# Optimization experiments

Measured on AMD Instinct MI355X. Metric: run time of the kernel, lower is better.

## Reference

```python
import jax, jax.numpy as jnp
import numpy as np

H = 8  # heads hardcoded in LightGFormer


def layernorm(x, g, b, eps=1e-5):
    m = x.mean(-1, keepdims=True)
    v = ((x - m) ** 2).mean(-1, keepdims=True)
    return (x - m) / jnp.sqrt(v + eps) * g + b


def setup_inputs() -> dict:
    key = jax.random.key(0)
    B, N, D, L = 16, 512, 256, 4
    Dff = 4 * D
    ks = jax.random.split(key, 12)

    def w(k, shape, scale=0.02):
        return jax.random.normal(k, shape, jnp.float32) * scale

    return {
        "input": w(ks[0], (B, N, D), 1.0),
        "input_v": w(ks[1], (B, N, D), 1.0),
        "pos_emb": w(ks[2], (N, D)),
        "Wq": w(ks[3], (L, D, D)), "bq": jnp.zeros((L, D), jnp.float32),
        "Wk": w(ks[4], (L, D, D)), "bk": jnp.zeros((L, D), jnp.float32),
        "Wv": w(ks[5], (L, D, D)), "bv": jnp.zeros((L, D), jnp.float32),
        "Wo": w(ks[6], (L, D, D)), "bo": jnp.zeros((L, D), jnp.float32),
        "W1": w(ks[7], (L, D, Dff)), "b1": jnp.zeros((L, Dff), jnp.float32),
        "W2": w(ks[8], (L, Dff // 2, D // 2)), "b2": jnp.zeros((L, D // 2), jnp.float32),
        "g1": jnp.ones((L, D), jnp.float32), "be1": jnp.zeros((L, D), jnp.float32),
        "g2": jnp.ones((L, D), jnp.float32), "be2": jnp.zeros((L, D), jnp.float32),
        "gf": jnp.ones((D,), jnp.float32), "bf": jnp.zeros((D,), jnp.float32),
        "mask": jax.random.randint(ks[9], (N, N), 0, 2) > 0,
    }


def reference(input, input_v, pos_emb, Wq, bq, Wk, bk, Wv, bv, Wo, bo,
              W1, b1, W2, b2, g1, be1, g2, be2, gf, bf, mask):
    B, N, D = input.shape
    L = Wq.shape[0]
    dk = D // H
    scale = 1.0 / float(np.sqrt(dk))

    x = input + pos_emb[None]       # learned positional encoding
    xv = input_v + pos_emb[None]    # values stream (never updated across layers)

    for i in range(L):
        # --- self-attention: queries/keys from x, values from xv ---
        q = (x @ Wq[i] + bq[i]).reshape(B, N, H, dk)
        k = (x @ Wk[i] + bk[i]).reshape(B, N, H, dk)
        v = (xv @ Wv[i] + bv[i]).reshape(B, N, H, dk)
        att = jnp.einsum('bqhd,bkhd->bhqk', q, k) * scale
        if i % 2 == 1:  # odd layers use the mask (Lightformer alternation)
            att = jnp.where(mask[None, None], -jnp.inf, att)
        att = jax.nn.softmax(att, axis=-1)
        o = jnp.einsum('bhqk,bkhd->bqhd', att, v).reshape(B, N, D)
        o = o @ Wo[i] + bo[i]
        x = layernorm(x + o, g1[i], be1[i])
        # --- FFN with grouped second linear: [.., 2, 2D] @ [2D, D/2] ---
        h = jax.nn.gelu(x @ W1[i] + b1[i], approximate=False)
        h = (h.reshape(B, N, 2, 2 * D) @ W2[i] + b2[i]).reshape(B, N, D)
        x = layernorm(x + h, g2[i], be2[i])

    x = layernorm(x, gf, bf)  # final attention_norm
    return x
```

## Files before the change

### kernel.cpp

```cpp
#include <hip/hip_runtime.h>
#include <hip/hip_bf16.h>
#include <math.h>

#define BDIM 16
#define NSEQ 512
#define DMODEL 256
#define NLAYER 4
#define NHEAD 8
#define DK 32
#define DFF 1024
#define BN (BDIM * NSEQ)
#define ND (NSEQ * DMODEL)

typedef __bf16 bf16x8 __attribute__((ext_vector_type(8)));
typedef float floatx4 __attribute__((ext_vector_type(4)));
typedef unsigned uint32x2 __attribute__((ext_vector_type(2)));

static __device__ __forceinline__ unsigned short f2bf(float f) {
    unsigned u = __float_as_uint(f);
    unsigned r = (u + 0x7FFFu + ((u >> 16) & 1u)) >> 16;
    return (unsigned short)r;
}

static __device__ __forceinline__ void async_ld16(const unsigned short* g,
                                                  unsigned short* l) {
    __builtin_amdgcn_global_load_lds(
        (const __attribute__((address_space(1))) unsigned int*)g,
        (__attribute__((address_space(3))) unsigned int*)l, 16, 0, 0);
}

static __device__ __forceinline__ float gelu_f(float c) {
    float u = 0.7978845608028654f * (c + 0.044715f * c * c * c);
    return c * (1.f / (1.f + __expf(-2.f * u)));
}

__global__ void conv_all_kernel(const float* __restrict__ Wq, const float* __restrict__ Wk,
                                const float* __restrict__ Wv, const float* __restrict__ Wo,
                                const float* __restrict__ W1, const float* __restrict__ W2,
                                const int* __restrict__ mask,
                                unsigned short* __restrict__ wqT, unsigned short* __restrict__ wkT,
                                unsigned short* __restrict__ wvT, unsigned short* __restrict__ woT,
                                unsigned short* __restrict__ w1T, unsigned short* __restrict__ w2T,
                                unsigned* __restrict__ bits) {
    int blk = blockIdx.x, tid = threadIdx.x;
    if (blk < 4096) {
        int i = blk * 256 + tid;
        int sel = i >> 18;
        int j = i & 262143;
        int l = j >> 16, rem = j & 65535, kk = rem >> 8, n = rem & 255;
        const float* src = sel == 0 ? Wq : sel == 1 ? Wk : sel == 2 ? Wv : Wo;
        unsigned short* dst = sel == 0 ? wqT : sel == 1 ? wkT : sel == 2 ? wvT : woT;
        dst[(size_t)l * 65536 + n * 256 + kk] = f2bf(src[j]);
    } else if (blk < 8192) {
        int i = (blk - 4096) * 256 + tid;
        int l = i >> 18, rem = i & 262143, kk = rem >> 10, n = rem & 1023;
        w1T[(size_t)l * 262144 + (size_t)n * 256 + kk] = f2bf(W1[i]);
    } else if (blk < 9216) {
        int j = (blk - 8192) * 256 + tid;
        int l = j >> 16, rem = j & 65535, kk = rem >> 7, n = rem & 127;
        w2T[(size_t)l * 65536 + (size_t)n * 512 + kk] = f2bf(W2[j]);
    } else {
        int w = (blk - 9216) * 256 + tid;
        int r = w >> 4, wi = w & 15;
        const int* src = mask + r * NSEQ + wi * 32;
        unsigned acc = 0;
#pragma unroll
        for (int j = 0; j < 32; j++) acc |= (src[j] != 0 ? 1u : 0u) << j;
        bits[w] = acc;
    }
}

__global__ void add_pos_kernel(const float* __restrict__ in,
                               const float* __restrict__ inv,
                               const float* __restrict__ pos,
                               float* __restrict__ x,
                               unsigned short* __restrict__ xb,
                               unsigned short* __restrict__ xvb,
                               int total) {
    int i = blockIdx.x * blockDim.x + threadIdx.x;
    if (i < total) {
        float pe = pos[i % ND];
        float a = in[i] + pe;
        float b = inv[i] + pe;
        x[i] = a;
        xb[i] = f2bf(a);
        xvb[i] = f2bf(b);
    }
}

__global__ __launch_bounds__(256) void qkv_mfma_kernel(
        const unsigned short* __restrict__ xb,
        const unsigned short* __restrict__ xvb,
        const unsigned short* __restrict__ WqT, const unsigned short* __restrict__ WkT,
        const unsigned short* __restrict__ WvT,
        const float* __restrict__ bq, const float* __restrict__ bk,
        const float* __restrict__ bv,
        unsigned short* __restrict__ qo, unsigned short* __restrict__ ko,
        unsigned short* __restrict__ vo) {
    int proj = blockIdx.x >> 1;
    const unsigned short* A  = (proj == 2) ? xvb : xb;
    const unsigned short* Bt = (proj == 0) ? WqT : (proj == 1) ? WkT : WvT;
    const float* bias        = (proj == 0) ? bq  : (proj == 1) ? bk  : bv;
    unsigned short* Cb       = (proj == 0) ? qo  : (proj == 1) ? ko  : vo;
    float qscale = (proj == 0) ? 0.17677669529663687f : 1.f;

    __shared__ unsigned short As[2][128 * 32];
    __shared__ unsigned short Bs[2][128 * 32];
    int tid = threadIdx.x;
    int wave = tid >> 6, lane = tid & 63;
    int rowBase = blockIdx.y * 128, colBase = (blockIdx.x & 1) * 128;
    int m0w = (wave & 1) * 64, n0w = (wave >> 1) * 64;
    int lr = lane & 15, quad = lane >> 4;
    int qx = quad ^ (lr & 3);

    floatx4 acc[4][4];
#pragma unroll
    for (int mi = 0; mi < 4; mi++)
#pragma unroll
        for (int nj = 0; nj < 4; nj++) acc[mi][nj] = (floatx4)0.0f;

    auto stage = [&](int kt, int b) {
#pragma unroll
        for (int t = 0; t < 2; t++) {
            int idx = t * 256 + tid;
            int row = idx >> 2, kv8 = ((idx ^ row) & 3) * 8;
            async_ld16(A + (size_t)(rowBase + row) * DMODEL + kt * 32 + kv8, &As[b][idx * 8]);
            async_ld16(Bt + (size_t)(colBase + row) * DMODEL + kt * 32 + kv8, &Bs[b][idx * 8]);
        }
    };
    stage(0, 0);

    for (int kt = 0; kt < 8; kt++) {
        int cur = kt & 1;
        bool more = (kt < 7);
        if (more) stage(kt + 1, cur ^ 1);
        if (more) asm volatile("s_waitcnt vmcnt(4)");
        else      asm volatile("s_waitcnt vmcnt(0)");
        __builtin_amdgcn_s_barrier();
        __builtin_amdgcn_sched_barrier(0);
        bf16x8 af[4], bfr[4];
#pragma unroll
        for (int mi = 0; mi < 4; mi++)
            af[mi] = *(const bf16x8*)&As[cur][(m0w + mi * 16 + lr) * 32 + qx * 8];
#pragma unroll
        for (int nj = 0; nj < 4; nj++)
            bfr[nj] = *(const bf16x8*)&Bs[cur][(n0w + nj * 16 + lr) * 32 + qx * 8];
#pragma unroll
        for (int mi = 0; mi < 4; mi++)
#pragma unroll
            for (int nj = 0; nj < 4; nj++)
                acc[mi][nj] = __builtin_amdgcn_mfma_f32_16x16x32_bf16(
                    af[mi], bfr[nj], acc[mi][nj], 0, 0, 0);
        if (more) {
            asm volatile("s_waitcnt lgkmcnt(0)");
            __builtin_amdgcn_sched_barrier(0);
            __builtin_amdgcn_s_barrier();
        }
    }

#pragma unroll
    for (int mi = 0; mi < 4; mi++) {
#pragma unroll
        for (int r = 0; r < 4; r++) {
            int grow = rowBase + m0w + mi * 16 + quad * 4 + r;
#pragma unroll
            for (int nj = 0; nj < 4; nj++) {
                int gcol = colBase + n0w + nj * 16 + lr;
                float c = (acc[mi][nj][r] + bias[gcol]) * qscale;
                size_t off = ((size_t)((grow >> 9) * 8 + (gcol >> 5)) << 14)
                           + (size_t)(grow & 511) * 32 + (gcol & 31);
                Cb[off] = f2bf(c);
            }
        }
    }
}

__global__ __launch_bounds__(256) void gemm_mfma_kernel(
        const unsigned short* __restrict__ A,
        const unsigned short* __restrict__ Bt,
        const float* __restrict__ bias,
        unsigned short* __restrict__ Cb,
        int M, int K, int N, int act) {
    __shared__ unsigned short As[2][128 * 32];
    __shared__ unsigned short Bs[2][128 * 32];
    int tid = threadIdx.x;
    int wave = tid >> 6, lane = tid & 63;
    int rowBase = blockIdx.y * 128, colBase = blockIdx.x * 128;
    int m0w = (wave & 1) * 64, n0w = (wave >> 1) * 64;
    int lr = lane & 15, quad = lane >> 4;
    int qx = quad ^ (lr & 3);
    int NK = K >> 5;

    floatx4 acc[4][4];
#pragma unroll
    for (int mi = 0; mi < 4; mi++)
#pragma unroll
        for (int nj = 0; nj < 4; nj++) acc[mi][nj] = (floatx4)0.0f;

    auto stage = [&](int kt, int b) {
#pragma unroll
        for (int t = 0; t < 2; t++) {
            int idx = t * 256 + tid;
            int row = idx >> 2, kv8 = ((idx ^ row) & 3) * 8;
            async_ld16(A + (size_t)(rowBase + row) * K + kt * 32 + kv8, &As[b][idx * 8]);
            async_ld16(Bt + (size_t)(colBase + row) * K + kt * 32 + kv8, &Bs[b][idx * 8]);
        }
    };
    stage(0, 0);

    for (int kt = 0; kt < NK; kt++) {
        int cur = kt & 1;
        bool more = (kt < NK - 1);
        if (more) stage(kt + 1, cur ^ 1);
        if (more) asm volatile("s_waitcnt vmcnt(4)");
        else      asm volatile("s_waitcnt vmcnt(0)");
        __builtin_amdgcn_s_barrier();
        __builtin_amdgcn_sched_barrier(0);
        bf16x8 af[4], bfr[4];
#pragma unroll
        for (int mi = 0; mi < 4; mi++)
            af[mi] = *(const bf16x8*)&As[cur][(m0w + mi * 16 + lr) * 32 + qx * 8];
#pragma unroll
        for (int nj = 0; nj < 4; nj++)
            bfr[nj] = *(const bf16x8*)&Bs[cur][(n0w + nj * 16 + lr) * 32 + qx * 8];
#pragma unroll
        for (int mi = 0; mi < 4; mi++)
#pragma unroll
            for (int nj = 0; nj < 4; nj++)
                acc[mi][nj] = __builtin_amdgcn_mfma_f32_16x16x32_bf16(
                    af[mi], bfr[nj], acc[mi][nj], 0, 0, 0);
        if (more) {
            asm volatile("s_waitcnt lgkmcnt(0)");
            __builtin_amdgcn_sched_barrier(0);
            __builtin_amdgcn_s_barrier();
        }
    }

#pragma unroll
    for (int mi = 0; mi < 4; mi++) {
#pragma unroll
        for (int r = 0; r < 4; r++) {
            int grow = rowBase + m0w + mi * 16 + quad * 4 + r;
#pragma unroll
            for (int nj = 0; nj < 4; nj++) {
                int gcol = colBase + n0w + nj * 16 + lr;
                float c = acc[mi][nj][r] + bias[gcol];
                if (act) c = gelu_f(c);
                Cb[(size_t)grow * N + gcol] = f2bf(c);
            }
        }
    }
}

__global__ __launch_bounds__(64) void wo_ln_kernel(
        const unsigned short* __restrict__ A,
        const unsigned short* __restrict__ Bt,
        const float* __restrict__ bias,
        const float* __restrict__ g, const float* __restrict__ be,
        float* __restrict__ xf, unsigned short* __restrict__ xb) {
    __shared__ unsigned short As[2][16 * 32];
    __shared__ unsigned short Bs[2][256 * 32];
    int tid = threadIdx.x;
    int l16 = tid & 15, quad = tid >> 4;
    int rowBase = blockIdx.x * 16;
    int qx = quad ^ (l16 & 3);

    floatx4 acc[16];
#pragma unroll
    for (int t = 0; t < 16; t++) acc[t] = (floatx4)0.0f;

    auto stage = [&](int kt, int b) {
        {
            int row = tid >> 2, kv8 = ((tid ^ row) & 3) * 8;
            async_ld16(A + (size_t)(rowBase + row) * 256 + kt * 32 + kv8, &As[b][tid * 8]);
        }
#pragma unroll
        for (int t = 0; t < 16; t++) {
            int idx = t * 64 + tid;
            int row = idx >> 2, kv8 = ((idx ^ row) & 3) * 8;
            async_ld16(Bt + (size_t)row * 256 + kt * 32 + kv8, &Bs[b][idx * 8]);
        }
    };
    stage(0, 0);

    for (int kt = 0; kt < 8; kt++) {
        int cur = kt & 1;
        bool more = (kt < 7);
        if (more) stage(kt + 1, cur ^ 1);
        if (more) asm volatile("s_waitcnt vmcnt(17)");
        else      asm volatile("s_waitcnt vmcnt(0)");
        __builtin_amdgcn_sched_barrier(0);
        bf16x8 af = *(const bf16x8*)&As[cur][l16 * 32 + qx * 8];
#pragma unroll
        for (int t = 0; t < 16; t++) {
            bf16x8 bfr = *(const bf16x8*)&Bs[cur][(t * 16 + l16) * 32 + qx * 8];
            acc[t] = __builtin_amdgcn_mfma_f32_16x16x32_bf16(af, bfr, acc[t], 0, 0, 0);
        }
    }

    float bcol[16], gc[16], bec[16];
#pragma unroll
    for (int t = 0; t < 16; t++) {
        int c = t * 16 + l16;
        bcol[t] = bias[c]; gc[t] = g[c]; bec[t] = be[c];
    }
#pragma unroll
    for (int r = 0; r < 4; r++) {
        int grow = rowBase + quad * 4 + r;
        float v[16], s = 0.f, s2 = 0.f;
#pragma unroll
        for (int t = 0; t < 16; t++) {
            int c = t * 16 + l16;
            float val = acc[t][r] + bcol[t] + xf[(size_t)grow * 256 + c];
            v[t] = val; s += val; s2 += val * val;
        }
#pragma unroll
        for (int off = 1; off <= 8; off <<= 1) {
            s += __shfl_xor(s, off);
            s2 += __shfl_xor(s2, off);
        }
        float mean = s * (1.f / 256.f);
        float var = s2 * (1.f / 256.f) - mean * mean;
        float rstd = rsqrtf(var + 1e-5f);
#pragma unroll
        for (int t = 0; t < 16; t++) {
            int c = t * 16 + l16;
            float o = (v[t] - mean) * rstd * gc[t] + bec[t];
            xf[(size_t)grow * 256 + c] = o;
            xb[(size_t)grow * 256 + c] = f2bf(o);
        }
    }
}

__global__ __launch_bounds__(128) void ffn2_ln_kernel(
        const unsigned short* __restrict__ A,
        const unsigned short* __restrict__ Bt,
        const float* __restrict__ bias,
        const float* __restrict__ g, const float* __restrict__ be,
        float* __restrict__ xf, unsigned short* __restrict__ xb) {
    __shared__ unsigned short As[2][64 * 32];
    __shared__ unsigned short Bs[2][128 * 32];
    __shared__ float redS[64][2], redQ[64][2];
    int tid = threadIdx.x;
    int wave = tid >> 6, lane = tid & 63, l16 = lane & 15, quad = lane >> 4;
    int rowBase = blockIdx.x * 64;
    int n0w = wave * 64;
    int qx = quad ^ (l16 & 3);

    floatx4 acc[4][4];
#pragma unroll
    for (int mi = 0; mi < 4; mi++)
#pragma unroll
        for (int nj = 0; nj < 4; nj++) acc[mi][nj] = (floatx4)0.0f;

    auto stage = [&](int kt, int b) {
#pragma unroll
        for (int t = 0; t < 2; t++) {
            int idx = t * 128 + tid;
            int row = idx >> 2, kv8 = ((idx ^ row) & 3) * 8;
            async_ld16(A + (size_t)(rowBase + row) * 512 + kt * 32 + kv8, &As[b][idx * 8]);
        }
#pragma unroll
        for (int t = 0; t < 4; t++) {
            int idx = t * 128 + tid;
            int row = idx >> 2, kv8 = ((idx ^ row) & 3) * 8;
            async_ld16(Bt + (size_t)row * 512 + kt * 32 + kv8, &Bs[b][idx * 8]);
        }
    };
    stage(0, 0);

    for (int kt = 0; kt < 16; kt++) {
        int cur = kt & 1;
        bool more = (kt < 15);
        if (more) stage(kt + 1, cur ^ 1);
        if (more) asm volatile("s_waitcnt vmcnt(6)");
        else      asm volatile("s_waitcnt vmcnt(0)");
        __builtin_amdgcn_s_barrier();
        __builtin_amdgcn_sched_barrier(0);
        bf16x8 af[4], bfr[4];
#pragma unroll
        for (int mi = 0; mi < 4; mi++)
            af[mi] = *(const bf16x8*)&As[cur][(mi * 16 + l16) * 32 + qx * 8];
#pragma unroll
        for (int nj = 0; nj < 4; nj++)
            bfr[nj] = *(const bf16x8*)&Bs[cur][(n0w + nj * 16 + l16) * 32 + qx * 8];
#pragma unroll
        for (int mi = 0; mi < 4; mi++)
#pragma unroll
            for (int nj = 0; nj < 4; nj++)
                acc[mi][nj] = __builtin_amdgcn_mfma_f32_16x16x32_bf16(
                    af[mi], bfr[nj], acc[mi][nj], 0, 0, 0);
        if (more) {
            asm volatile("s_waitcnt lgkmcnt(0)");
            __builtin_amdgcn_sched_barrier(0);
            __builtin_amdgcn_s_barrier();
        }
    }

#pragma unroll
    for (int mi = 0; mi < 4; mi++) {
#pragma unroll
        for (int r = 0; r < 4; r++) {
            int row = mi * 16 + quad * 4 + r;
            int grow = rowBase + row;
            int token = grow >> 1, dbase = (grow & 1) * 128;
            float s = 0.f, s2 = 0.f;
#pragma unroll
            for (int nj = 0; nj < 4; nj++) {
                int gcol = n0w + nj * 16 + l16;
                float val = acc[mi][nj][r] + bias[gcol]
                          + xf[(size_t)token * 256 + dbase + gcol];
                acc[mi][nj][r] = val;
                s += val; s2 += val * val;
            }
#pragma unroll
            for (int off = 1; off <= 8; off <<= 1) {
                s += __shfl_xor(s, off);
                s2 += __shfl_xor(s2, off);
            }
            if (l16 == 0) { redS[row][wave] = s; redQ[row][wave] = s2; }
        }
    }
    __syncthreads();

#pragma unroll
    for (int mi = 0; mi < 4; mi++) {
#pragma unroll
        for (int r = 0; r < 4; r++) {
            int row = mi * 16 + quad * 4 + r;
            int grow = rowBase + row;
            int token = grow >> 1, dbase = (grow & 1) * 128;
            float ts = redS[row][0] + redS[row][1] + redS[row ^ 1][0] + redS[row ^ 1][1];
            float tq = redQ[row][0] + redQ[row][1] + redQ[row ^ 1][0] + redQ[row ^ 1][1];
            float mean = ts * (1.f / 256.f);
            float var = tq * (1.f / 256.f) - mean * mean;
            float rstd = rsqrtf(var + 1e-5f);
#pragma unroll
            for (int nj = 0; nj < 4; nj++) {
                int gcol = n0w + nj * 16 + l16;
                int d = dbase + gcol;
                float o = (acc[mi][nj][r] - mean) * rstd * g[d] + be[d];
                xf[(size_t)token * 256 + d] = o;
                xb[(size_t)token * 256 + d] = f2bf(o);
            }
        }
    }
}

__global__ __launch_bounds__(256, 4) void attn_mfma_kernel(
        const unsigned short* __restrict__ q, const unsigned short* __restrict__ k,
        const unsigned short* __restrict__ v, unsigned short* __restrict__ o,
        const unsigned* __restrict__ mbits_g, int use_mask) {
    int bid = blockIdx.x;
    int qg = bid >> 7;
    int bh = bid & 127;
    int h = bh & 7, b = bh >> 3;
    int tid = threadIdx.x;

    __shared__ unsigned short Vs[2][NSEQ * 16];

    const unsigned short* kbase = k + (size_t)(b * 8 + h) * (NSEQ * DK);
    const unsigned short* vbase = v + (size_t)(b * 8 + h) * (NSEQ * DK);

#pragma unroll
    for (int db = 0; db < 2; db++) {
#pragma unroll
        for (int t = 0; t < 4; t++) {
            int c = t * 256 + tid;
            int kk = c >> 1, half = c & 1;
            async_ld16(vbase + (size_t)kk * 32 + db * 16 + half * 8,
                       &Vs[db][c * 8]);
        }
    }

    int wave = tid >> 6, lane = tid & 63, l16 = lane & 15, quad = lane >> 4;
    int qbase = qg * 64 + wave * 16;

    bf16x8 qf = *(const bf16x8*)(q + ((size_t)(b * 8 + h) * NSEQ + qbase + l16) * 32 + quad * 8);

    unsigned mw[16];
    if (use_mask) {
        const uint4* mr = (const uint4*)(mbits_g + (size_t)(qbase + l16) * 16);
#pragma unroll
        for (int w = 0; w < 4; w++) *(uint4*)&mw[w * 4] = mr[w];
    } else {
#pragma unroll
        for (int w = 0; w < 16; w++) mw[w] = 0;
    }
    __syncthreads();

    unsigned va0 = (unsigned)(size_t)&Vs[0][0] + (unsigned)(lane * 8);
    unsigned va1 = (unsigned)(size_t)&Vs[1][0] + (unsigned)(lane * 8);

    const unsigned short* kfrag = kbase + (size_t)l16 * DK + quad * 8;

    floatx4 oT0 = (floatx4)0.f, oT1 = (floatx4)0.f;
    float m_run = -INFINITY, l_part = 0.f;

    uint32x2 t00, t01, t10, t11;
#define TR_ISSUE(cc)                                                      \
    asm volatile("ds_read_b64_tr_b16 %0, %4\n\t"                          \
                 "ds_read_b64_tr_b16 %1, %4 offset:512\n\t"               \
                 "ds_read_b64_tr_b16 %2, %5\n\t"                          \
                 "ds_read_b64_tr_b16 %3, %5 offset:512"                   \
                 : "=&v"(t00), "=&v"(t01), "=&v"(t10), "=&v"(t11)         \
                 : "v"(va0 + (unsigned)((cc) * 1024)),                    \
                   "v"(va1 + (unsigned)((cc) * 1024)))
    TR_ISSUE(0);

    bf16x8 k0 = *(const bf16x8*)(kfrag);
    bf16x8 k1 = *(const bf16x8*)(kfrag + 16 * DK);

#pragma unroll
    for (int c = 0; c < 16; c++) {
        floatx4 s0 = __builtin_amdgcn_mfma_f32_16x16x32_bf16(k0, qf, (floatx4)0.f, 0, 0, 0);
        floatx4 s1 = __builtin_amdgcn_mfma_f32_16x16x32_bf16(k1, qf, (floatx4)0.f, 0, 0, 0);

        bf16x8 k0n, k1n;
        if (c < 15) {
            k0n = *(const bf16x8*)(kfrag + (size_t)((c + 1) * 32) * DK);
            k1n = *(const bf16x8*)(kfrag + (size_t)((c + 1) * 32 + 16) * DK);
        }

        float sv[8];
#pragma unroll
        for (int r = 0; r < 4; r++) { sv[r] = s0[r]; sv[4 + r] = s1[r]; }
        if (use_mask) {
            unsigned wb = mw[c];
#pragma unroll
            for (int r = 0; r < 4; r++) {
                if ((wb >> (quad * 4 + r)) & 1) sv[r] = -INFINITY;
                if ((wb >> (16 + quad * 4 + r)) & 1) sv[4 + r] = -INFINITY;
            }
        }
        float mx = fmaxf(fmaxf(fmaxf(sv[0], sv[1]), fmaxf(sv[2], sv[3])),
                         fmaxf(fmaxf(sv[4], sv[5]), fmaxf(sv[6], sv[7])));
        mx = fmaxf(mx, __shfl_xor(mx, 16));
        mx = fmaxf(mx, __shfl_xor(mx, 32));
        if (!__all(mx <= m_run)) {
            float mnew = fmaxf(m_run, mx);
            float corr = (m_run == mnew) ? 1.f : __expf(m_run - mnew);
            l_part *= corr;
            oT0 *= corr; oT1 *= corr;
            m_run = mnew;
        }
        float p[8];
#pragma unroll
        for (int j = 0; j < 8; j++) {
            float e = __expf(sv[j] - m_run);
            p[j] = (sv[j] > -INFINITY) ? e : 0.f;
            l_part += p[j];
        }
        union { bf16x8 v8; unsigned u[4]; } pf;
#pragma unroll
        for (int j = 0; j < 4; j++)
            asm("v_cvt_pk_bf16_f32 %0, %1, %2"
                : "=v"(pf.u[j]) : "v"(p[2 * j]), "v"(p[2 * j + 1]));

        asm volatile("s_waitcnt lgkmcnt(0)");
        __builtin_amdgcn_sched_barrier(0);
        union { bf16x8 v8; uint32x2 u[2]; } av0, av1;
        av0.u[0] = t00; av0.u[1] = t01;
        av1.u[0] = t10; av1.u[1] = t11;

        oT0 = __builtin_amdgcn_mfma_f32_16x16x32_bf16(av0.v8, pf.v8, oT0, 0, 0, 0);
        oT1 = __builtin_amdgcn_mfma_f32_16x16x32_bf16(av1.v8, pf.v8, oT1, 0, 0, 0);
        if (c < 15) TR_ISSUE(c + 1);
        k0 = k0n; k1 = k1n;
    }
#undef TR_ISSUE

    float l = l_part;
    l += __shfl_xor(l, 16);
    l += __shfl_xor(l, 32);
    float invl = (l > 0.f) ? 1.f / l : 0.f;

    unsigned short* orow = o + ((size_t)(b * NSEQ + qbase + l16)) * DMODEL + h * DK;
#pragma unroll
    for (int r = 0; r < 4; r++) {
        orow[quad * 4 + r]      = f2bf(oT0[r] * invl);
        orow[16 + quad * 4 + r] = f2bf(oT1[r] * invl);
    }
}

__global__ __launch_bounds__(256) void final_ln_kernel(
        const float* __restrict__ a,
        const float* __restrict__ g, const float* __restrict__ be,
        float* __restrict__ out) {
    int t = blockIdx.x;
    int d = threadIdx.x;
    size_t idx = (size_t)t * DMODEL + d;
    float v = a[idx];
    float s = v, s2 = v * v;
#pragma unroll
    for (int off = 32; off; off >>= 1) {
        s  += __shfl_xor(s, off);
        s2 += __shfl_xor(s2, off);
    }
    __shared__ float ws1[4], ws2[4];
    int wid = d >> 6;
    if ((d & 63) == 0) { ws1[wid] = s; ws2[wid] = s2; }
    __syncthreads();
    s  = ws1[0] + ws1[1] + ws1[2] + ws1[3];
    s2 = ws2[0] + ws2[1] + ws2[2] + ws2[3];
    float mean = s * (1.f / DMODEL);
    float var = s2 * (1.f / DMODEL) - mean * mean;
    float rstd = rsqrtf(var + 1e-5f);
    out[idx] = (v - mean) * rstd * g[d] + be[d];
}

extern "C" void kernel_launch(void* const* d_in, const int* in_sizes, int n_in,
                              void* d_out, int out_size, void* d_ws, size_t ws_size,
                              hipStream_t stream) {
    const float* input  = (const float*)d_in[0];
    const float* inputv = (const float*)d_in[1];
    const float* pos    = (const float*)d_in[2];
    const float* Wq = (const float*)d_in[3];
    const float* bq = (const float*)d_in[4];
    const float* Wk = (const float*)d_in[5];
    const float* bk = (const float*)d_in[6];
    const float* Wv = (const float*)d_in[7];
    const float* bv = (const float*)d_in[8];
    const float* Wo = (const float*)d_in[9];
    const float* bo = (const float*)d_in[10];
    const float* W1 = (const float*)d_in[11];
    const float* b1 = (const float*)d_in[12];
    const float* W2 = (const float*)d_in[13];
    const float* b2 = (const float*)d_in[14];
    const float* g1 = (const float*)d_in[15];
    const float* be1 = (const float*)d_in[16];
    const float* g2 = (const float*)d_in[17];
    const float* be2 = (const float*)d_in[18];
    const float* gf = (const float*)d_in[19];
    const float* bff = (const float*)d_in[20];
    const int* mask = (const int*)d_in[21];

    float* out = (float*)d_out;

    char* wsb = (char*)d_ws;
    float* x_f  = (float*)(wsb + ((size_t)0 << 20));
    unsigned short* x_b  = (unsigned short*)(wsb + ((size_t)8 << 20));
    unsigned short* xv_b = (unsigned short*)(wsb + ((size_t)12 << 20));
    unsigned short* qb_b = (unsigned short*)(wsb + ((size_t)16 << 20));
    unsigned short* kb_b = (unsigned short*)(wsb + ((size_t)20 << 20));
    unsigned short* vb_b = (unsigned short*)(wsb + ((size_t)24 << 20));
    unsigned short* ab_b = (unsigned short*)(wsb + ((size_t)28 << 20));
    unsigned short* h_b  = qb_b;
    unsigned short* wqT = (unsigned short*)(wsb + ((size_t)32 << 20));
    unsigned short* wkT = wqT + (size_t)4 * 65536;
    unsigned short* wvT = wkT + (size_t)4 * 65536;
    unsigned short* woT = wvT + (size_t)4 * 65536;
    unsigned short* w1T = woT + (size_t)4 * 65536;
    unsigned short* w2T = w1T + (size_t)4 * 262144;
    unsigned* mbits = (unsigned*)(wsb + ((size_t)37 << 20));

    const size_t TOK = (size_t)BN * DMODEL;

    conv_all_kernel<<<9248, 256, 0, stream>>>(Wq, Wk, Wv, Wo, W1, W2, mask,
                                              wqT, wkT, wvT, woT, w1T, w2T, mbits);
    add_pos_kernel<<<(int)((TOK + 255) / 256), 256, 0, stream>>>(
        input, inputv, pos, x_f, x_b, xv_b, (int)TOK);

    for (int i = 0; i < NLAYER; i++) {
        const unsigned short* WqT_i = wqT + (size_t)i * 65536;
        const unsigned short* WkT_i = wkT + (size_t)i * 65536;
        const unsigned short* WvT_i = wvT + (size_t)i * 65536;
        const unsigned short* WoT_i = woT + (size_t)i * 65536;
        const unsigned short* W1T_i = w1T + (size_t)i * 262144;
        const unsigned short* W2T_i = w2T + (size_t)i * 65536;

        qkv_mfma_kernel<<<dim3(6, 64), 256, 0, stream>>>(
            x_b, xv_b, WqT_i, WkT_i, WvT_i,
            bq + i * DMODEL, bk + i * DMODEL, bv + i * DMODEL,
            qb_b, kb_b, vb_b);

        attn_mfma_kernel<<<BDIM * NHEAD * 8, 256, 0, stream>>>(
            qb_b, kb_b, vb_b, ab_b, mbits, (i & 1));

        wo_ln_kernel<<<BN / 16, 64, 0, stream>>>(
            ab_b, WoT_i, bo + i * DMODEL,
            g1 + i * DMODEL, be1 + i * DMODEL, x_f, x_b);

        gemm_mfma_kernel<<<dim3(8, 64), 256, 0, stream>>>(
            x_b, W1T_i, b1 + i * DFF, h_b, BN, DMODEL, DFF, 1);

        ffn2_ln_kernel<<<(2 * BN) / 64, 128, 0, stream>>>(
            h_b, W2T_i, b2 + i * (DMODEL / 2),
            g2 + i * DMODEL, be2 + i * DMODEL, x_f, x_b);
    }

    final_ln_kernel<<<BN, DMODEL, 0, stream>>>(x_f, gf, bff, out);
}
```

Measured before the change: 462.4 us.

## Fuse Wo+LN1, FFN1+GELU, FFN2+LN2 and final LN into one per-layer kernel

Replaces the Wo+LayerNorm kernel, the FFN1 GEMM with GELU, and the grouped FFN2+LayerNorm kernel with a single kernel per layer. Each block handles 32 tokens and keeps the post-attention activations and the 1024-wide hidden layer in LDS, so the hidden tensor is never written to or read from global memory. The final LayerNorm is folded into the last layer's epilogue. In exchange, each block streams every weight matrix for only 32 rows, which lowers weight reuse, and the large LDS footprint with only 256 blocks may limit occupancy.

```diff
diff --git a/kernel.cpp b/kernel.cpp
--- a/kernel.cpp
+++ b/kernel.cpp
@@ -20,6 +20,9 @@
     unsigned u = __float_as_uint(f);
     unsigned r = (u + 0x7FFFu + ((u >> 16) & 1u)) >> 16;
     return (unsigned short)r;
+}
+static __device__ __forceinline__ float bf2f(unsigned short u) {
+    return __uint_as_float(((unsigned)u) << 16);
 }
 
 static __device__ __forceinline__ void async_ld16(const unsigned short* g,
@@ -175,275 +178,353 @@
     }
 }
 
-__global__ __launch_bounds__(256) void gemm_mfma_kernel(
-        const unsigned short* __restrict__ A,
-        const unsigned short* __restrict__ Bt,
-        const float* __restrict__ bias,
-        unsigned short* __restrict__ Cb,
-        int M, int K, int N, int act) {
-    __shared__ unsigned short As[2][128 * 32];
-    __shared__ unsigned short Bs[2][128 * 32];
+__global__ __launch_bounds__(256) void ffn_fused_kernel(
+        const unsigned short* __restrict__ Aab,
+        const unsigned short* __restrict__ woT,
+        const unsigned short* __restrict__ w1T,
+        const unsigned short* __restrict__ w2T,
+        const float* __restrict__ bo,
+        const float* __restrict__ g1, const float* __restrict__ be1,
+        const float* __restrict__ b1,
+        const float* __restrict__ b2,
+        const float* __restrict__ g2, const float* __restrict__ be2,
+        const float* __restrict__ gf, const float* __restrict__ bf_,
+        float* __restrict__ xf, unsigned short* __restrict__ xb,
+        float* __restrict__ outF, int finalize) {
+    __shared__ unsigned short Ab[8][1024];
+    __shared__ unsigned short X1[8][1024];
+    __shared__ unsigned short Hh[16][1024];
+    __shared__ unsigned short Bst[16384];
+    __shared__ float redA[32][4], redB[32][4];
+    __shared__ float redC[32][4], redD[32][4];
+    __shared__ float redE[32][4], redF[32][4];
+
     int tid = threadIdx.x;
-    int wave = tid >> 6, lane = tid & 63;
-    int rowBase = blockIdx.y * 128, colBase = blockIdx.x * 128;
-    int m0w = (wave & 1) * 64, n0w = (wave >> 1) * 64;
-    int lr = lane & 15, quad = lane >> 4;
-    int qx = quad ^ (lr & 3);
-    int NK = K >> 5;
-
-    floatx4 acc[4][4];
-#pragma unroll
-    for (int mi = 0; mi < 4; mi++)
-#pragma unroll
-        for (int nj = 0; nj < 4; nj++) acc[mi][nj] = (floatx4)0.0f;
-
-    auto stage = [&](int kt, int b) {
-#pragma unroll
-        for (int t = 0; t < 2; t++) {
-            int idx = t * 256 + tid;
-            int row = idx >> 2, kv8 = ((idx ^ row) & 3) * 8;
-            async_ld16(A + (size_t)(rowBase + row) * K + kt * 32 + kv8, &As[b][idx * 8]);
-            async_ld16(Bt + (size_t)(colBase + row) * K + kt * 32 + kv8, &Bs[b][idx * 8]);
+    int w = tid >> 6, lane = tid & 63, l16 = lane & 15, quad = lane >> 4;
+    int qx = quad ^ (l16 & 3);
+    int rowBase = blockIdx.x * 32;
+    unsigned short* Bw = Bst + w * 4096;
+
+    float b1r[2][4][2];
+#pragma unroll
+    for (int g = 0; g < 2; g++)
+#pragma unroll
+        for (int nc = 0; nc < 4; nc++)
+#pragma unroll
+            for (int cj = 0; cj < 2; cj++) {
+                b1r[g][nc][cj] = b1[g * 512 + w * 128 + nc * 32 + cj * 16 + l16];
+                asm volatile("" :: "v"(b1r[g][nc][cj]));
+            }
+
+#pragma unroll
+    for (int t = 0; t < 4; t++) {
+        int idx = t * 256 + tid;
+        int kt = idx >> 7;
+        int r  = (idx >> 2) & 31;
+        int ch = idx & 3, chx = ch ^ (r & 3);
+        async_ld16(Aab + (size_t)(rowBase + r) * 256 + kt * 32 + chx * 8,
+                   ((unsigned short*)Ab) + idx * 8);
+    }
+
+    floatx4 accA[2][4];
+#pragma unroll
+    for (int mi = 0; mi < 2; mi++)
+#pragma unroll
+        for (int nj = 0; nj < 4; nj++) accA[mi][nj] = (floatx4)0.0f;
+
+    auto stageA = [&](int kt, int b) {
+#pragma unroll
+        for (int t = 0; t < 4; t++) {
+            int idx = t * 64 + lane;
+            int r = idx >> 2, ch = idx & 3, chx = ch ^ (r & 3);
+            async_ld16(woT + (size_t)(w * 64 + r) * 256 + kt * 32 + chx * 8,
+                       Bw + b * 2048 + idx * 8);
         }
     };
-    stage(0, 0);
-
-    for (int kt = 0; kt < NK; kt++) {
+    stageA(0, 0);
+    stageA(1, 1);
+    asm volatile("s_waitcnt vmcnt(4)");
+    __builtin_amdgcn_sched_barrier(0);
+    __builtin_amdgcn_s_barrier();
+    __builtin_amdgcn_sched_barrier(0);
+
+#pragma unroll
+    for (int kt = 0; kt < 8; kt++) {
         int cur = kt & 1;
-        bool more = (kt < NK - 1);
-        if (more) stage(kt + 1, cur ^ 1);
-        if (more) asm volatile("s_waitcnt vmcnt(4)");
-        else      asm volatile("s_waitcnt vmcnt(0)");
-        __builtin_amdgcn_s_barrier();
+        if (kt < 7) asm volatile("s_waitcnt vmcnt(4)");
+        else        asm volatile("s_waitcnt vmcnt(0)");
         __builtin_amdgcn_sched_barrier(0);
-        bf16x8 af[4], bfr[4];
-#pragma unroll
-        for (int mi = 0; mi < 4; mi++)
-            af[mi] = *(const bf16x8*)&As[cur][(m0w + mi * 16 + lr) * 32 + qx * 8];
+        bf16x8 af[2], bfr[4];
+#pragma unroll
+        for (int mi = 0; mi < 2; mi++)
+            af[mi] = *(const bf16x8*)&Ab[kt][(mi * 16 + l16) * 32 + qx * 8];
 #pragma unroll
         for (int nj = 0; nj < 4; nj++)
-            bfr[nj] = *(const bf16x8*)&Bs[cur][(n0w + nj * 16 + lr) * 32 + qx * 8];
-#pragma unroll
-        for (int mi = 0; mi < 4; mi++)
+            bfr[nj] = *(const bf16x8*)(Bw + cur * 2048 + (nj * 16 + l16) * 32 + qx * 8);
+#pragma unroll
+        for (int mi = 0; mi < 2; mi++)
 #pragma unroll
             for (int nj = 0; nj < 4; nj++)
-                acc[mi][nj] = __builtin_amdgcn_mfma_f32_16x16x32_bf16(
-                    af[mi], bfr[nj], acc[mi][nj], 0, 0, 0);
-        if (more) {
+                accA[mi][nj] = __builtin_amdgcn_mfma_f32_16x16x32_bf16(
+                    af[mi], bfr[nj], accA[mi][nj], 0, 0, 0);
+        if (kt < 6) {
             asm volatile("s_waitcnt lgkmcnt(0)");
             __builtin_amdgcn_sched_barrier(0);
-            __builtin_amdgcn_s_barrier();
-        }
-    }
-
-#pragma unroll
-    for (int mi = 0; mi < 4; mi++) {
-#pragma unroll
-        for (int r = 0; r < 4; r++) {
-            int grow = rowBase + m0w + mi * 16 + quad * 4 + r;
-#pragma unroll
-            for (int nj = 0; nj < 4; nj++) {
-                int gcol = colBase + n0w + nj * 16 + lr;
-                float c = acc[mi][nj][r] + bias[gcol];
-                if (act) c = gelu_f(c);
-                Cb[(size_t)grow * N + gcol] = f2bf(c);
-            }
-        }
-    }
-}
-
-__global__ __launch_bounds__(64) void wo_ln_kernel(
-        const unsigned short* __restrict__ A,
-        const unsigned short* __restrict__ Bt,
-        const float* __restrict__ bias,
-        const float* __restrict__ g, const float* __restrict__ be,
-        float* __restrict__ xf, unsigned short* __restrict__ xb) {
-    __shared__ unsigned short As[2][16 * 32];
-    __shared__ unsigned short Bs[2][256 * 32];
-    int tid = threadIdx.x;
-    int l16 = tid & 15, quad = tid >> 4;
-    int rowBase = blockIdx.x * 16;
-    int qx = quad ^ (l16 & 3);
-
-    floatx4 acc[16];
-#pragma unroll
-    for (int t = 0; t < 16; t++) acc[t] = (floatx4)0.0f;
-
-    auto stage = [&](int kt, int b) {
-        {
-            int row = tid >> 2, kv8 = ((tid ^ row) & 3) * 8;
-            async_ld16(A + (size_t)(rowBase + row) * 256 + kt * 32 + kv8, &As[b][tid * 8]);
-        }
-#pragma unroll
-        for (int t = 0; t < 16; t++) {
-            int idx = t * 64 + tid;
-            int row = idx >> 2, kv8 = ((idx ^ row) & 3) * 8;
-            async_ld16(Bt + (size_t)row * 256 + kt * 32 + kv8, &Bs[b][idx * 8]);
-        }
-    };
-    stage(0, 0);
-
-    for (int kt = 0; kt < 8; kt++) {
-        int cur = kt & 1;
-        bool more = (kt < 7);
-        if (more) stage(kt + 1, cur ^ 1);
-        if (more) asm volatile("s_waitcnt vmcnt(17)");
-        else      asm volatile("s_waitcnt vmcnt(0)");
-        __builtin_amdgcn_sched_barrier(0);
-        bf16x8 af = *(const bf16x8*)&As[cur][l16 * 32 + qx * 8];
-#pragma unroll
-        for (int t = 0; t < 16; t++) {
-            bf16x8 bfr = *(const bf16x8*)&Bs[cur][(t * 16 + l16) * 32 + qx * 8];
-            acc[t] = __builtin_amdgcn_mfma_f32_16x16x32_bf16(af, bfr, acc[t], 0, 0, 0);
-        }
-    }
-
-    float bcol[16], gc[16], bec[16];
-#pragma unroll
-    for (int t = 0; t < 16; t++) {
-        int c = t * 16 + l16;
-        bcol[t] = bias[c]; gc[t] = g[c]; bec[t] = be[c];
-    }
-#pragma unroll
-    for (int r = 0; r < 4; r++) {
-        int grow = rowBase + quad * 4 + r;
-        float v[16], s = 0.f, s2 = 0.f;
-#pragma unroll
-        for (int t = 0; t < 16; t++) {
-            int c = t * 16 + l16;
-            float val = acc[t][r] + bcol[t] + xf[(size_t)grow * 256 + c];
-            v[t] = val; s += val; s2 += val * val;
-        }
-#pragma unroll
-        for (int off = 1; off <= 8; off <<= 1) {
-            s += __shfl_xor(s, off);
-            s2 += __shfl_xor(s2, off);
-        }
-        float mean = s * (1.f / 256.f);
-        float var = s2 * (1.f / 256.f) - mean * mean;
-        float rstd = rsqrtf(var + 1e-5f);
-#pragma unroll
-        for (int t = 0; t < 16; t++) {
-            int c = t * 16 + l16;
-            float o = (v[t] - mean) * rstd * gc[t] + bec[t];
-            xf[(size_t)grow * 256 + c] = o;
-            xb[(size_t)grow * 256 + c] = f2bf(o);
-        }
-    }
-}
-
-__global__ __launch_bounds__(128) void ffn2_ln_kernel(
-        const unsigned short* __restrict__ A,
-        const unsigned short* __restrict__ Bt,
-        const float* __restrict__ bias,
-        const float* __restrict__ g, const float* __restrict__ be,
-        float* __restrict__ xf, unsigned short* __restrict__ xb) {
-    __shared__ unsigned short As[2][64 * 32];
-    __shared__ unsigned short Bs[2][128 * 32];
-    __shared__ float redS[64][2], redQ[64][2];
-    int tid = threadIdx.x;
-    int wave = tid >> 6, lane = tid & 63, l16 = lane & 15, quad = lane >> 4;
-    int rowBase = blockIdx.x * 64;
-    int n0w = wave * 64;
-    int qx = quad ^ (l16 & 3);
-
-    floatx4 acc[4][4];
-#pragma unroll
-    for (int mi = 0; mi < 4; mi++)
-#pragma unroll
-        for (int nj = 0; nj < 4; nj++) acc[mi][nj] = (floatx4)0.0f;
-
-    auto stage = [&](int kt, int b) {
-#pragma unroll
-        for (int t = 0; t < 2; t++) {
-            int idx = t * 128 + tid;
-            int row = idx >> 2, kv8 = ((idx ^ row) & 3) * 8;
-            async_ld16(A + (size_t)(rowBase + row) * 512 + kt * 32 + kv8, &As[b][idx * 8]);
-        }
-#pragma unroll
-        for (int t = 0; t < 4; t++) {
-            int idx = t * 128 + tid;
-            int row = idx >> 2, kv8 = ((idx ^ row) & 3) * 8;
-            async_ld16(Bt + (size_t)row * 512 + kt * 32 + kv8, &Bs[b][idx * 8]);
-        }
-    };
-    stage(0, 0);
-
-    for (int kt = 0; kt < 16; kt++) {
-        int cur = kt & 1;
-        bool more = (kt < 15);
-        if (more) stage(kt + 1, cur ^ 1);
-        if (more) asm volatile("s_waitcnt vmcnt(6)");
-        else      asm volatile("s_waitcnt vmcnt(0)");
-        __builtin_amdgcn_s_barrier();
-        __builtin_amdgcn_sched_barrier(0);
-        bf16x8 af[4], bfr[4];
-#pragma unroll
-        for (int mi = 0; mi < 4; mi++)
-            af[mi] = *(const bf16x8*)&As[cur][(mi * 16 + l16) * 32 + qx * 8];
-#pragma unroll
-        for (int nj = 0; nj < 4; nj++)
-            bfr[nj] = *(const bf16x8*)&Bs[cur][(n0w + nj * 16 + l16) * 32 + qx * 8];
-#pragma unroll
-        for (int mi = 0; mi < 4; mi++)
-#pragma unroll
-            for (int nj = 0; nj < 4; nj++)
-                acc[mi][nj] = __builtin_amdgcn_mfma_f32_16x16x32_bf16(
-                    af[mi], bfr[nj], acc[mi][nj], 0, 0, 0);
-        if (more) {
-            asm volatile("s_waitcnt lgkmcnt(0)");
-            __builtin_amdgcn_sched_barrier(0);
-            __builtin_amdgcn_s_barrier();
-        }
-    }
-
-#pragma unroll
-    for (int mi = 0; mi < 4; mi++) {
+            stageA(kt + 2, cur);
+        }
+    }
+
+#pragma unroll
+    for (int mi = 0; mi < 2; mi++)
 #pragma unroll
         for (int r = 0; r < 4; r++) {
             int row = mi * 16 + quad * 4 + r;
-            int grow = rowBase + row;
-            int token = grow >> 1, dbase = (grow & 1) * 128;
             float s = 0.f, s2 = 0.f;
 #pragma unroll
             for (int nj = 0; nj < 4; nj++) {
-                int gcol = n0w + nj * 16 + l16;
-                float val = acc[mi][nj][r] + bias[gcol]
-                          + xf[(size_t)token * 256 + dbase + gcol];
-                acc[mi][nj][r] = val;
-                s += val; s2 += val * val;
+                int col = w * 64 + nj * 16 + l16;
+                float v = accA[mi][nj][r] + bo[col]
+                        + xf[(size_t)(rowBase + row) * 256 + col];
+                accA[mi][nj][r] = v; s += v; s2 += v * v;
             }
 #pragma unroll
             for (int off = 1; off <= 8; off <<= 1) {
                 s += __shfl_xor(s, off);
                 s2 += __shfl_xor(s2, off);
             }
-            if (l16 == 0) { redS[row][wave] = s; redQ[row][wave] = s2; }
-        }
-    }
+            if (l16 == 0) { redA[row][w] = s; redB[row][w] = s2; }
+        }
     __syncthreads();
-
-#pragma unroll
-    for (int mi = 0; mi < 4; mi++) {
+#pragma unroll
+    for (int mi = 0; mi < 2; mi++)
 #pragma unroll
         for (int r = 0; r < 4; r++) {
             int row = mi * 16 + quad * 4 + r;
-            int grow = rowBase + row;
-            int token = grow >> 1, dbase = (grow & 1) * 128;
-            float ts = redS[row][0] + redS[row][1] + redS[row ^ 1][0] + redS[row ^ 1][1];
-            float tq = redQ[row][0] + redQ[row][1] + redQ[row ^ 1][0] + redQ[row ^ 1][1];
+            float ts = redA[row][0] + redA[row][1] + redA[row][2] + redA[row][3];
+            float tq = redB[row][0] + redB[row][1] + redB[row][2] + redB[row][3];
             float mean = ts * (1.f / 256.f);
             float var = tq * (1.f / 256.f) - mean * mean;
             float rstd = rsqrtf(var + 1e-5f);
 #pragma unroll
             for (int nj = 0; nj < 4; nj++) {
-                int gcol = n0w + nj * 16 + l16;
-                int d = dbase + gcol;
-                float o = (acc[mi][nj][r] - mean) * rstd * g[d] + be[d];
-                xf[(size_t)token * 256 + d] = o;
-                xb[(size_t)token * 256 + d] = f2bf(o);
-            }
-        }
+                int col = w * 64 + nj * 16 + l16;
+                float o = (accA[mi][nj][r] - mean) * rstd * g1[col] + be1[col];
+                int c5 = col & 31;
+                X1[col >> 5][row * 32 + (((c5 >> 3) ^ (row & 3)) << 3) + (c5 & 7)] = f2bf(o);
+            }
+        }
+    __syncthreads();
+
+    floatx4 y[2][2][2];
+#pragma unroll
+    for (int g = 0; g < 2; g++)
+#pragma unroll
+        for (int mi = 0; mi < 2; mi++)
+#pragma unroll
+            for (int cj = 0; cj < 2; cj++) y[g][mi][cj] = (floatx4)0.0f;
+
+#pragma unroll
+    for (int g = 0; g < 2; g++) {
+        auto stageB = [&](int s) {
+            int nc = s >> 3, kt = s & 7, b = s & 3;
+#pragma unroll
+            for (int t = 0; t < 2; t++) {
+                int idx = t * 64 + lane;
+                int r = idx >> 2, ch = idx & 3, chx = ch ^ (r & 3);
+                async_ld16(w1T + (size_t)(g * 512 + w * 128 + nc * 32 + r) * 256
+                               + kt * 32 + chx * 8,
+                           Bw + b * 1024 + idx * 8);
+            }
+        };
+        stageB(0); stageB(1); stageB(2); stageB(3);
+        floatx4 accB[2][2];
+#pragma unroll
+        for (int s = 0; s < 32; s++) {
+            if ((s & 7) == 0) {
+#pragma unroll
+                for (int mi = 0; mi < 2; mi++)
+#pragma unroll
+                    for (int cj = 0; cj < 2; cj++) accB[mi][cj] = (floatx4)0.0f;
+            }
+            if (s < 29)      asm volatile("s_waitcnt vmcnt(6)");
+            else if (s == 29) asm volatile("s_waitcnt vmcnt(4)");
+            else if (s == 30) asm volatile("s_waitcnt vmcnt(2)");
+            else              asm volatile("s_waitcnt vmcnt(0)");
+            __builtin_amdgcn_sched_barrier(0);
+            int kt = s & 7, buf = s & 3;
+            bf16x8 af[2], bfr[2];
+#pragma unroll
+            for (int mi = 0; mi < 2; mi++)
+                af[mi] = *(const bf16x8*)&X1[kt][(mi * 16 + l16) * 32 + qx * 8];
+#pragma unroll
+            for (int cj = 0; cj < 2; cj++)
+                bfr[cj] = *(const bf16x8*)(Bw + buf * 1024 + (cj * 16 + l16) * 32 + qx * 8);
+#pragma unroll
+            for (int mi = 0; mi < 2; mi++)
+#pragma unroll
+                for (int cj = 0; cj < 2; cj++)
+                    accB[mi][cj] = __builtin_amdgcn_mfma_f32_16x16x32_bf16(
+                        af[mi], bfr[cj], accB[mi][cj], 0, 0, 0);
+            if (s < 28) {
+                asm volatile("s_waitcnt lgkmcnt(0)");
+                __builtin_amdgcn_sched_barrier(0);
+                stageB(s + 4);
+            }
+            if ((s & 7) == 7) {
+                int nc = s >> 3;
+#pragma unroll
+                for (int mi = 0; mi < 2; mi++)
+#pragma unroll
+                    for (int cj = 0; cj < 2; cj++)
+#pragma unroll
+                        for (int r = 0; r < 4; r++) {
+                            int row = mi * 16 + quad * 4 + r;
+                            int kcol = w * 128 + nc * 32 + cj * 16 + l16;
+                            float hv = gelu_f(accB[mi][cj][r] + b1r[g][nc][cj]);
+                            int c5 = kcol & 31;
+                            Hh[kcol >> 5][row * 32 + (((c5 >> 3) ^ (row & 3)) << 3) + (c5 & 7)]
+                                = f2bf(hv);
+                        }
+            }
+        }
+        __syncthreads();
+
+        auto stageC = [&](int kt) {
+            int b = kt & 3;
+#pragma unroll
+            for (int t = 0; t < 2; t++) {
+                int idx = t * 64 + lane;
+                int r = idx >> 2, ch = idx & 3, chx = ch ^ (r & 3);
+                async_ld16(w2T + (size_t)(w * 32 + r) * 512 + kt * 32 + chx * 8,
+                           Bw + b * 1024 + idx * 8);
+            }
+        };
+        stageC(0); stageC(1); stageC(2); stageC(3);
+#pragma unroll
+        for (int kt = 0; kt < 16; kt++) {
+            if (kt < 13)      asm volatile("s_waitcnt vmcnt(6)");
+            else if (kt == 13) asm volatile("s_waitcnt vmcnt(4)");
+            else if (kt == 14) asm volatile("s_waitcnt vmcnt(2)");
+            else               asm volatile("s_waitcnt vmcnt(0)");
+            __builtin_amdgcn_sched_barrier(0);
+            int buf = kt & 3;
+            bf16x8 af[2], bfr[2];
+#pragma unroll
+            for (int mi = 0; mi < 2; mi++)
+                af[mi] = *(const bf16x8*)&Hh[kt][(mi * 16 + l16) * 32 + qx * 8];
+#pragma unroll
+            for (int cj = 0; cj < 2; cj++)
+                bfr[cj] = *(const bf16x8*)(Bw + buf * 1024 + (cj * 16 + l16) * 32 + qx * 8);
+#pragma unroll
+            for (int mi = 0; mi < 2; mi++)
+#pragma unroll
+                for (int cj = 0; cj < 2; cj++)
+                    y[g][mi][cj] = __builtin_amdgcn_mfma_f32_16x16x32_bf16(
+                        af[mi], bfr[cj], y[g][mi][cj], 0, 0, 0);
+            if (kt < 12) {
+                asm volatile("s_waitcnt lgkmcnt(0)");
+                __builtin_amdgcn_sched_barrier(0);
+                stageC(kt + 4);
+            }
+        }
+        if (g == 0) __syncthreads();
+    }
+
+#pragma unroll
+    for (int mi = 0; mi < 2; mi++)
+#pragma unroll
+        for (int r = 0; r < 4; r++) {
+            int row = mi * 16 + quad * 4 + r;
+            float s = 0.f, s2 = 0.f;
+#pragma unroll
+            for (int g = 0; g < 2; g++)
+#pragma unroll
+                for (int cj = 0; cj < 2; cj++) {
+                    int cc = w * 32 + cj * 16 + l16;
+                    int col = g * 128 + cc;
+                    int c5 = col & 31;
+                    float x1v = bf2f(X1[col >> 5][row * 32 +
+                                     (((c5 >> 3) ^ (row & 3)) << 3) + (c5 & 7)]);
+                    float v = y[g][mi][cj][r] + b2[cc] + x1v;
+                    y[g][mi][cj][r] = v; s += v; s2 += v * v;
+                }
+#pragma unroll
+            for (int off = 1; off <= 8; off <<= 1) {
+                s += __shfl_xor(s, off);
+                s2 += __shfl_xor(s2, off);
+            }
+            if (l16 == 0) { redC[row][w] = s; redD[row][w] = s2; }
+        }
+    __syncthreads();
+
+    if (!finalize) {
+#pragma unroll
+        for (int mi = 0; mi < 2; mi++)
+#pragma unroll
+            for (int r = 0; r < 4; r++) {
+                int row = mi * 16 + quad * 4 + r;
+                float ts = redC[row][0] + redC[row][1] + redC[row][2] + redC[row][3];
+                float tq = redD[row][0] + redD[row][1] + redD[row][2] + redD[row][3];
+                float mean = ts * (1.f / 256.f);
+                float var = tq * (1.f / 256.f) - mean * mean;
+                float rstd = rsqrtf(var + 1e-5f);
+#pragma unroll
+                for (int g = 0; g < 2; g++)
+#pragma unroll
+                    for (int cj = 0; cj < 2; cj++) {
+                        int col = g * 128 + w * 32 + cj * 16 + l16;
+                        float o = (y[g][mi][cj][r] - mean) * rstd * g2[col] + be2[col];
+                        xf[(size_t)(rowBase + row) * 256 + col] = o;
+                        xb[(size_t)(rowBase + row) * 256 + col] = f2bf(o);
+                    }
+            }
+    } else {
+#pragma unroll
+        for (int mi = 0; mi < 2; mi++)
+#pragma unroll
+            for (int r = 0; r < 4; r++) {
+                int row = mi * 16 + quad * 4 + r;
+                float ts = redC[row][0] + redC[row][1] + redC[row][2] + redC[row][3];
+                float tq = redD[row][0] + redD[row][1] + redD[row][2] + redD[row][3];
+                float mean = ts * (1.f / 256.f);
+                float var = tq * (1.f / 256.f) - mean * mean;
+                float rstd = rsqrtf(var + 1e-5f);
+                float s3 = 0.f, q3 = 0.f;
+#pragma unroll
+                for (int g = 0; g < 2; g++)
+#pragma unroll
+                    for (int cj = 0; cj < 2; cj++) {
+                        int col = g * 128 + w * 32 + cj * 16 + l16;
+                        float o = (y[g][mi][cj][r] - mean) * rstd * g2[col] + be2[col];
+                        y[g][mi][cj][r] = o; s3 += o; q3 += o * o;
+                    }
+#pragma unroll
+                for (int off = 1; off <= 8; off <<= 1) {
+                    s3 += __shfl_xor(s3, off);
+                    q3 += __shfl_xor(q3, off);
+                }
+                if (l16 == 0) { redE[row][w] = s3; redF[row][w] = q3; }
+            }
+        __syncthreads();
+#pragma unroll
+        for (int mi = 0; mi < 2; mi++)
+#pragma unroll
+            for (int r = 0; r < 4; r++) {
+                int row = mi * 16 + quad * 4 + r;
+                float ts = redE[row][0] + redE[row][1] + redE[row][2] + redE[row][3];
+                float tq = redF[row][0] + redF[row][1] + redF[row][2] + redF[row][3];
+                float mean = ts * (1.f / 256.f);
+                float var = tq * (1.f / 256.f) - mean * mean;
+                float rstd = rsqrtf(var + 1e-5f);
+#pragma unroll
+                for (int g = 0; g < 2; g++)
+#pragma unroll
+                    for (int cj = 0; cj < 2; cj++) {
+                        int col = g * 128 + w * 32 + cj * 16 + l16;
+                        outF[(size_t)(rowBase + row) * 256 + col]
+                            = (y[g][mi][cj][r] - mean) * rstd * gf[col] + bf_[col];
+                    }
+            }
     }
 }
 
@@ -581,32 +662,6 @@
         orow[quad * 4 + r]      = f2bf(oT0[r] * invl);
         orow[16 + quad * 4 + r] = f2bf(oT1[r] * invl);
     }
-}
-
-__global__ __launch_bounds__(256) void final_ln_kernel(
-        const float* __restrict__ a,
-        const float* __restrict__ g, const float* __restrict__ be,
-        float* __restrict__ out) {
-    int t = blockIdx.x;
-    int d = threadIdx.x;
-    size_t idx = (size_t)t * DMODEL + d;
-    float v = a[idx];
-    float s = v, s2 = v * v;
-#pragma unroll
-    for (int off = 32; off; off >>= 1) {
-        s  += __shfl_xor(s, off);
-        s2 += __shfl_xor(s2, off);
-    }
-    __shared__ float ws1[4], ws2[4];
-    int wid = d >> 6;
-    if ((d & 63) == 0) { ws1[wid] = s; ws2[wid] = s2; }
-    __syncthreads();
-    s  = ws1[0] + ws1[1] + ws1[2] + ws1[3];
-    s2 = ws2[0] + ws2[1] + ws2[2] + ws2[3];
-    float mean = s * (1.f / DMODEL);
-    float var = s2 * (1.f / DMODEL) - mean * mean;
-    float rstd = rsqrtf(var + 1e-5f);
-    out[idx] = (v - mean) * rstd * g[d] + be[d];
 }
 
 extern "C" void kernel_launch(void* const* d_in, const int* in_sizes, int n_in,
@@ -645,7 +700,6 @@
     unsigned short* kb_b = (unsigned short*)(wsb + ((size_t)20 << 20));
     unsigned short* vb_b = (unsigned short*)(wsb + ((size_t)24 << 20));
     unsigned short* ab_b = (unsigned short*)(wsb + ((size_t)28 << 20));
-    unsigned short* h_b  = qb_b;
     unsigned short* wqT = (unsigned short*)(wsb + ((size_t)32 << 20));
     unsigned short* wkT = wqT + (size_t)4 * 65536;
     unsigned short* wvT = wkT + (size_t)4 * 65536;
@@ -677,17 +731,11 @@
         attn_mfma_kernel<<<BDIM * NHEAD * 8, 256, 0, stream>>>(
             qb_b, kb_b, vb_b, ab_b, mbits, (i & 1));
 
-        wo_ln_kernel<<<BN / 16, 64, 0, stream>>>(
-            ab_b, WoT_i, bo + i * DMODEL,
-            g1 + i * DMODEL, be1 + i * DMODEL, x_f, x_b);
-
-        gemm_mfma_kernel<<<dim3(8, 64), 256, 0, stream>>>(
-            x_b, W1T_i, b1 + i * DFF, h_b, BN, DMODEL, DFF, 1);
-
-        ffn2_ln_kernel<<<(2 * BN) / 64, 128, 0, stream>>>(
-            h_b, W2T_i, b2 + i * (DMODEL / 2),
-            g2 + i * DMODEL, be2 + i * DMODEL, x_f, x_b);
-    }
-
-    final_ln_kernel<<<BN, DMODEL, 0, stream>>>(x_f, gf, bff, out);
-}
+        ffn_fused_kernel<<<BN / 32, 256, 0, stream>>>(
+            ab_b, WoT_i, W1T_i, W2T_i,
+            bo + i * DMODEL, g1 + i * DMODEL, be1 + i * DMODEL,
+            b1 + i * DFF, b2 + i * (DMODEL / 2),
+            g2 + i * DMODEL, be2 + i * DMODEL,
+            gf, bff, x_f, x_b, out, (i == NLAYER - 1) ? 1 : 0);
+    }
+}
```

After: 476.0 us. 2.9% more time.
